# Performance work log

Measured on AMD Instinct MI355X. Metric: run time of the kernel, lower is better.

The kernel has to match this reference:

```python
import jax, jax.numpy as jnp
import numpy as np

HID = 150

def _lstm_layer(x, Wih, Whh, bih, bhh):
    # x: [T, D] -> [T, HID]; PyTorch gate order i, f, g, o
    b = bih + bhh
    xg = x @ Wih.T + b  # precompute input contribution: [T, 4H]
    def step(carry, xg_t):
        h, c = carry
        g = xg_t + h @ Whh.T
        i, f, gg, o = jnp.split(g, 4)
        i = jax.nn.sigmoid(i); f = jax.nn.sigmoid(f)
        gg = jnp.tanh(gg); o = jax.nn.sigmoid(o)
        c = f * c + i * gg
        h = o * jnp.tanh(c)
        return (h, c), h
    init = (jnp.zeros((HID,), x.dtype), jnp.zeros((HID,), x.dtype))
    _, ys = jax.lax.scan(step, init, xg)
    return ys

def _bilstm(x, Wih, Whh, bih, bhh):
    # x: [T, D]; params stacked [L, 2, ...]
    out = x
    for l in range(Wih.shape[0]):
        fwd = _lstm_layer(out, Wih[l, 0], Whh[l, 0], bih[l, 0], bhh[l, 0])
        bwd = _lstm_layer(out[::-1], Wih[l, 1], Whh[l, 1], bih[l, 1], bhh[l, 1])[::-1]
        out = jnp.concatenate([fwd, bwd], axis=-1)  # [T, 2H]
    return out

def setup_inputs() -> dict:
    key = jax.random.key(0)
    ks = jax.random.split(key, 16)
    s = 0.1  # keep LSTM gates in a sane range
    return {
        "inputs_solv": jax.random.normal(ks[0], (1, 4096, 300), jnp.float32),
        "inputs_solu": jax.random.normal(ks[1], (1, 4096, 300), jnp.float32),
        "solv_Wih": jax.random.normal(ks[2], (2, 2, 600, 300), jnp.float32) * s,
        "solv_Whh": jax.random.normal(ks[3], (2, 2, 600, 150), jnp.float32) * s,
        "solv_bih": jax.random.normal(ks[4], (2, 2, 600), jnp.float32) * s,
        "solv_bhh": jax.random.normal(ks[5], (2, 2, 600), jnp.float32) * s,
        "solu_Wih": jax.random.normal(ks[6], (2, 2, 600, 300), jnp.float32) * s,
        "solu_Whh": jax.random.normal(ks[7], (2, 2, 600, 150), jnp.float32) * s,
        "solu_bih": jax.random.normal(ks[8], (2, 2, 600), jnp.float32) * s,
        "solu_bhh": jax.random.normal(ks[9], (2, 2, 600), jnp.float32) * s,
        "fc1_w": jax.random.normal(ks[10], (2000, 600), jnp.float32) * 0.02,
        "fc1_b": jax.random.normal(ks[11], (2000,), jnp.float32) * 0.02,
        "fc2_w": jax.random.normal(ks[12], (1, 2000), jnp.float32) * 0.02,
        "fc2_b": jax.random.normal(ks[13], (1,), jnp.float32) * 0.02,
    }

def reference(inputs_solv, inputs_solu, solv_Wih, solv_Whh, solv_bih, solv_bhh,
              solu_Wih, solu_Whh, solu_bih, solu_bhh, fc1_w, fc1_b, fc2_w, fc2_b):
    H = _bilstm(inputs_solv[0], solv_Wih, solv_Whh, solv_bih, solv_bhh)  # [Hs, 300]
    G = _bilstm(inputs_solu[0], solu_Wih, solu_Whh, solu_bih, solu_bhh)  # [Gs, 300]
    a_score = H @ G.T                      # fused version of the nested loop: [Hs, Gs]
    a = jax.nn.softmax(a_score, axis=1)
    P = a @ G                              # [Hs, 300]
    Q = a.T @ H                            # [Gs, 300]
    u = jnp.maximum(H, P)
    v = jnp.maximum(G, Q)
    inp = jnp.concatenate([u.sum(axis=0), v.sum(axis=0)], axis=0)  # [600]
    x = jax.nn.relu(inp @ fc1_w.T + fc1_b)
    return x @ fc2_w.T + fc2_b
```

## Files before the change

kernel.cpp:

```cpp
#include <hip/hip_runtime.h>
#include <hip/hip_fp16.h>
#include <cstddef>

#define T_LEN 4096
#define HID 150
#define G4 600
#define NC 300

typedef __attribute__((ext_vector_type(8))) short bf16x8;
typedef __attribute__((ext_vector_type(4))) float f32x4;

__device__ __forceinline__ void barrier_lgkm() {
  asm volatile("s_waitcnt lgkmcnt(0)\n\ts_barrier" ::: "memory");
}

__device__ __forceinline__ float fsig(float x) {
  return __builtin_amdgcn_rcpf(1.f + __expf(-x));
}
__device__ __forceinline__ float ftanh(float x) {
  float ax = fabsf(x);
  float e = __expf(2.f * ax);
  float t = 1.f - 2.f * __builtin_amdgcn_rcpf(e + 1.f);
  return copysignf(t, x);
}
__device__ __forceinline__ unsigned short f2bf(float f) {
  unsigned u = __builtin_bit_cast(unsigned, f);
  u += 0x7fff + ((u >> 16) & 1);
  return (unsigned short)(u >> 16);
}

__global__ __launch_bounds__(512, 2) void lstm_scan(
    const float* __restrict__ whh_solv, const float* __restrict__ whh_solu,
    const float* __restrict__ xg_base,
    float* __restrict__ out_solv, float* __restrict__ out_solu, int layer)
{
  __shared__ __align__(16) unsigned short h_bf[160];
  __shared__ float g_s[640];
  const int c = blockIdx.x;
  const int net = c >> 1, dir = c & 1;
  const float* Whh = (net ? whh_solu : whh_solv) + (size_t)(layer * 2 + dir) * (G4 * HID);
  const float* xg = xg_base + (size_t)c * T_LEN * G4;
  float* out = (net ? out_solu : out_solv) + dir * HID;
  const int tid = threadIdx.x;
  const int lane = tid & 63, wv = tid >> 6;
  const int lrow = lane & 15, lq = lane >> 4;

  bf16x8 bfr[5][5];
#pragma unroll
  for (int j = 0; j < 5; j++) {
    const int jrow = 16 * (wv + 8 * j) + lrow;
#pragma unroll
    for (int kk = 0; kk < 5; kk++) {
      bf16x8 b;
#pragma unroll
      for (int i = 0; i < 8; i++) {
        const int k = kk * 32 + lq * 8 + i;
        const float v = (jrow < G4 && k < HID) ? Whh[(size_t)jrow * HID + k] : 0.f;
        b[i] = (short)f2bf(v);
      }
      bfr[j][kk] = b;
    }
  }
  if (tid < 160) h_bf[tid] = 0;
  float cst = 0.f;
  float xr0 = 0.f, xr1 = 0.f, xr2 = 0.f, xr3 = 0.f;
  if (tid < HID) {
    const int t0 = dir ? (T_LEN - 1) : 0;
    const float* xgr = xg + (size_t)t0 * G4 + tid;
    xr0 = xgr[0]; xr1 = xgr[HID]; xr2 = xgr[2 * HID]; xr3 = xgr[3 * HID];
  }
  barrier_lgkm();

  for (int s = 0; s < T_LEN; s++) {
    const int t = dir ? (T_LEN - 1 - s) : s;
    bf16x8 af[5];
#pragma unroll
    for (int kk = 0; kk < 5; kk++) {
      bf16x8 a = {0, 0, 0, 0, 0, 0, 0, 0};
      if (lrow == 0) a = *(const bf16x8*)&h_bf[kk * 32 + lq * 8];
      af[kk] = a;
    }
    f32x4 acc[5];
#pragma unroll
    for (int j = 0; j < 5; j++) acc[j] = (f32x4){0.f, 0.f, 0.f, 0.f};
#pragma unroll
    for (int kk = 0; kk < 5; kk++)
#pragma unroll
      for (int j = 0; j < 5; j++)
        acc[j] = __builtin_amdgcn_mfma_f32_16x16x32_bf16(af[kk], bfr[j][kk], acc[j], 0, 0, 0);
    if (lane < 16) {
#pragma unroll
      for (int j = 0; j < 5; j++) g_s[16 * (wv + 8 * j) + lane] = acc[j][0];
    }
    barrier_lgkm();
    if (tid < HID) {
      const int n = tid;
      float gi = xr0 + g_s[n];
      float gf = xr1 + g_s[HID + n];
      float gg = xr2 + g_s[2 * HID + n];
      float go = xr3 + g_s[3 * HID + n];
      if (s + 1 < T_LEN) {
        const int tn = dir ? (T_LEN - 2 - s) : (s + 1);
        const float* xgr = xg + (size_t)tn * G4 + n;
        xr0 = xgr[0]; xr1 = xgr[HID]; xr2 = xgr[2 * HID]; xr3 = xgr[3 * HID];
      }
      const float iv = fsig(gi), fv = fsig(gf), gv = ftanh(gg), ov = fsig(go);
      cst = fv * cst + iv * gv;
      const float hv = ov * ftanh(cst);
      h_bf[n] = f2bf(hv);
      out[(size_t)t * NC + n] = hv;
    }
    barrier_lgkm();
  }
}

__device__ __forceinline__ float to_f(float v) { return v; }
__device__ __forceinline__ float to_f(__half v) { return __half2float(v); }

#define LP 68

template <int MODE, typename TA, int EPI>
__global__ void gemm_k(const TA* __restrict__ A, const float* __restrict__ B,
                       void* __restrict__ Cv, int M, int N, int K,
                       int lda, int ldb, int ldc,
                       const float* __restrict__ e0, const float* __restrict__ e1)
{
  __shared__ __align__(16) float As[16][LP];
  __shared__ __align__(16) float Bs[16][LP];
  const int tid = threadIdx.x;
  const int tx = tid & 15, ty = tid >> 4;
  const int m0 = blockIdx.y * 64, n0 = blockIdx.x * 64;
  float acc[4][4] = {};
  for (int kc = 0; kc < K; kc += 16) {
#pragma unroll
    for (int j = 0; j < 4; j++) {
      const int li = tid * 4 + j;
      int ml, kl;
      if (MODE == 2) { ml = li & 63; kl = li >> 6; }
      else           { ml = li >> 4; kl = li & 15; }
      const int m = m0 + ml, k = kc + kl;
      float v = 0.f;
      if (m < M && k < K)
        v = to_f(MODE == 2 ? A[(size_t)k * lda + m] : A[(size_t)m * lda + k]);
      As[kl][ml] = v;
    }
#pragma unroll
    for (int j = 0; j < 4; j++) {
      const int li = tid * 4 + j;
      int nl, kl;
      if (MODE == 0) { nl = li >> 4; kl = li & 15; }
      else           { nl = li & 63; kl = li >> 6; }
      const int n = n0 + nl, k = kc + kl;
      float v = 0.f;
      if (n < N && k < K)
        v = (MODE == 0) ? B[(size_t)n * ldb + k] : B[(size_t)k * ldb + n];
      Bs[kl][nl] = v;
    }
    __syncthreads();
#pragma unroll
    for (int kl = 0; kl < 16; kl++) {
      const float4 av = *(const float4*)&As[kl][ty * 4];
      const float4 bv = *(const float4*)&Bs[kl][tx * 4];
      const float aa[4] = {av.x, av.y, av.z, av.w};
      const float bb[4] = {bv.x, bv.y, bv.z, bv.w};
#pragma unroll
      for (int i = 0; i < 4; i++)
#pragma unroll
        for (int jj = 0; jj < 4; jj++)
          acc[i][jj] += aa[i] * bb[jj];
    }
    __syncthreads();
  }
#pragma unroll
  for (int i = 0; i < 4; i++) {
    const int m = m0 + ty * 4 + i;
    if (m >= M) continue;
#pragma unroll
    for (int j = 0; j < 4; j++) {
      const int n = n0 + tx * 4 + j;
      if (n >= N) continue;
      if (EPI == 0) {
        float v = acc[i][j];
        if (e0) v += e0[n] + e1[n];
        ((float*)Cv)[(size_t)m * ldc + n] = v;
      } else {
        const float v = __expf(acc[i][j] - e0[m]) * e1[m];
        ((__half*)Cv)[(size_t)m * ldc + n] = __float2half(v);
      }
    }
  }
}

__global__ void attn_stats(const float* __restrict__ Hm, const float* __restrict__ Gm,
                           float* __restrict__ pm, float* __restrict__ pl)
{
  __shared__ __align__(16) float As[16][LP];
  __shared__ __align__(16) float Bs[16][LP];
  const int tid = threadIdx.x;
  const int tx = tid & 15, ty = tid >> 4;
  const int m0 = blockIdx.y * 64;
  float rm[4], rl[4];
#pragma unroll
  for (int i = 0; i < 4; i++) { rm[i] = -3e38f; rl[i] = 0.f; }
  for (int nt = 0; nt < 8; nt++) {
    const int n0 = (blockIdx.x * 8 + nt) * 64;
    float acc[4][4] = {};
    for (int kc = 0; kc < NC; kc += 16) {
#pragma unroll
      for (int j = 0; j < 4; j++) {
        const int li = tid * 4 + j;
        const int ml = li >> 4, kl = li & 15;
        const int k = kc + kl;
        As[kl][ml] = (k < NC) ? Hm[(size_t)(m0 + ml) * NC + k] : 0.f;
        Bs[kl][ml] = (k < NC) ? Gm[(size_t)(n0 + ml) * NC + k] : 0.f;
      }
      __syncthreads();
#pragma unroll
      for (int kl = 0; kl < 16; kl++) {
        const float4 av = *(const float4*)&As[kl][ty * 4];
        const float4 bv = *(const float4*)&Bs[kl][tx * 4];
        const float aa[4] = {av.x, av.y, av.z, av.w};
        const float bb[4] = {bv.x, bv.y, bv.z, bv.w};
#pragma unroll
        for (int i = 0; i < 4; i++)
#pragma unroll
          for (int jj = 0; jj < 4; jj++)
            acc[i][jj] += aa[i] * bb[jj];
      }
      __syncthreads();
    }
#pragma unroll
    for (int i = 0; i < 4; i++) {
      const float mx = fmaxf(fmaxf(acc[i][0], acc[i][1]), fmaxf(acc[i][2], acc[i][3]));
      const float nm = fmaxf(rm[i], mx);
      const float s = __expf(acc[i][0] - nm) + __expf(acc[i][1] - nm) +
                      __expf(acc[i][2] - nm) + __expf(acc[i][3] - nm);
      rl[i] = rl[i] * __expf(rm[i] - nm) + s;
      rm[i] = nm;
    }
  }
  __syncthreads();
#pragma unroll
  for (int i = 0; i < 4; i++) { As[tx][ty * 4 + i] = rm[i]; Bs[tx][ty * 4 + i] = rl[i]; }
  __syncthreads();
  if (tid < 64) {
    float m = As[0][tid], l = Bs[0][tid];
#pragma unroll
    for (int c2 = 1; c2 < 16; c2++) {
      const float m2 = As[c2][tid], l2 = Bs[c2][tid];
      const float nm = fmaxf(m, m2);
      l = l * __expf(m - nm) + l2 * __expf(m2 - nm);
      m = nm;
    }
    pm[(size_t)(m0 + tid) * 8 + blockIdx.x] = m;
    pl[(size_t)(m0 + tid) * 8 + blockIdx.x] = l;
  }
}

__global__ void stats_combine(const float* __restrict__ pm, const float* __restrict__ pl,
                              float* __restrict__ mrow, float* __restrict__ invl)
{
  const int r = blockIdx.x * 256 + threadIdx.x;
  float m = -3e38f;
#pragma unroll
  for (int c2 = 0; c2 < 8; c2++) m = fmaxf(m, pm[r * 8 + c2]);
  float l = 0.f;
#pragma unroll
  for (int c2 = 0; c2 < 8; c2++) l += pl[r * 8 + c2] * __expf(pm[r * 8 + c2] - m);
  mrow[r] = m;
  invl[r] = 1.f / l;
}

__global__ void zero_inp(float* __restrict__ inp) {
  if (threadIdx.x < 600) inp[threadIdx.x] = 0.f;
}

__global__ void reduce_uv(const float* __restrict__ X, const float* __restrict__ Yp,
                          float* __restrict__ inp, int off)
{
  const int j = threadIdx.x;
  if (j >= NC) return;
  const int r0 = blockIdx.x * 128;
  float s = 0.f;
  for (int r = r0; r < r0 + 128; r++)
    s += fmaxf(X[(size_t)r * NC + j], Yp[(size_t)r * NC + j]);
  atomicAdd(&inp[off + j], s);
}

__global__ void fc1_k(const float* __restrict__ w1, const float* __restrict__ b1,
                      const float* __restrict__ inp, float* __restrict__ x)
{
  const int r = blockIdx.x * 256 + threadIdx.x;
  if (r >= 2000) return;
  float s = b1[r];
  const float* wr = w1 + (size_t)r * 600;
  for (int k = 0; k < 600; k++) s += wr[k] * inp[k];
  x[r] = fmaxf(s, 0.f);
}

__global__ void fc2_k(const float* __restrict__ x, const float* __restrict__ w2,
                      const float* __restrict__ b2, float* __restrict__ outp)
{
  const int tid = threadIdx.x;
  float s = 0.f;
  for (int i = tid; i < 2000; i += 256) s += x[i] * w2[i];
#pragma unroll
  for (int off = 32; off > 0; off >>= 1) s += __shfl_down(s, off);
  __shared__ float red[4];
  if ((tid & 63) == 0) red[tid >> 6] = s;
  __syncthreads();
  if (tid == 0) outp[0] = red[0] + red[1] + red[2] + red[3] + b2[0];
}

extern "C" void kernel_launch(void* const* d_in, const int* in_sizes, int n_in,
                              void* d_out, int out_size, void* d_ws, size_t ws_size,
                              hipStream_t stream)
{
  const float* in_solv  = (const float*)d_in[0];
  const float* in_solu  = (const float*)d_in[1];
  const float* solv_Wih = (const float*)d_in[2];
  const float* solv_Whh = (const float*)d_in[3];
  const float* solv_bih = (const float*)d_in[4];
  const float* solv_bhh = (const float*)d_in[5];
  const float* solu_Wih = (const float*)d_in[6];
  const float* solu_Whh = (const float*)d_in[7];
  const float* solu_bih = (const float*)d_in[8];
  const float* solu_bhh = (const float*)d_in[9];
  const float* fc1_w = (const float*)d_in[10];
  const float* fc1_b = (const float*)d_in[11];
  const float* fc2_w = (const float*)d_in[12];
  const float* fc2_b = (const float*)d_in[13];
  float* outp = (float*)d_out;
  float* ws = (float*)d_ws;

  constexpr size_t off_P   = 0;
  constexpr size_t off_Q   = 1228800;
  constexpr size_t off_inp = 2457600;
  constexpr size_t off_x   = 2458240;
  constexpr size_t off_pm  = 2460288;
  constexpr size_t off_pl  = 2493056;
  constexpr size_t off_mr  = 2525824;
  constexpr size_t off_il  = 2529920;
  constexpr size_t off_xg  = 2534016;
  constexpr size_t off_L0  = off_xg + (size_t)4 * 2457600;
  constexpr size_t off_HG  = off_L0 + (size_t)2 * 1228800;

  float* xg  = ws + off_xg;
  float* L0v = ws + off_L0;
  float* L0u = L0v + 1228800;
  float* Hb  = ws + off_HG;
  float* Gb  = Hb + 1228800;
  float* Pb  = ws + off_P;
  float* Qb  = ws + off_Q;
  float* inp = ws + off_inp;
  float* xf  = ws + off_x;
  float* pm  = ws + off_pm;
  float* pl  = ws + off_pl;
  float* mr  = ws + off_mr;
  float* il  = ws + off_il;
  __half* AH = (__half*)(ws + off_xg);

  for (int c = 0; c < 4; c++) {
    const int net = c >> 1, d = c & 1;
    const float* X   = net ? in_solu : in_solv;
    const float* Wih = (net ? solu_Wih : solv_Wih) + (size_t)d * (600 * 300);
    const float* bi  = (net ? solu_bih : solv_bih) + (size_t)d * 600;
    const float* bh  = (net ? solu_bhh : solv_bhh) + (size_t)d * 600;
    gemm_k<0, float, 0><<<dim3(10, 64), 256, 0, stream>>>(
        X, Wih, (void*)(xg + (size_t)c * 2457600), 4096, 600, 300, 300, 300, 600, bi, bh);
  }
  lstm_scan<<<4, 512, 0, stream>>>(solv_Whh, solu_Whh, xg, L0v, L0u, 0);

  for (int c = 0; c < 4; c++) {
    const int net = c >> 1, d = c & 1;
    const float* X   = net ? L0u : L0v;
    const float* Wih = (net ? solu_Wih : solv_Wih) + (size_t)(2 + d) * (600 * 300);
    const float* bi  = (net ? solu_bih : solv_bih) + (size_t)(2 + d) * 600;
    const float* bh  = (net ? solu_bhh : solv_bhh) + (size_t)(2 + d) * 600;
    gemm_k<0, float, 0><<<dim3(10, 64), 256, 0, stream>>>(
        X, Wih, (void*)(xg + (size_t)c * 2457600), 4096, 600, 300, 300, 300, 600, bi, bh);
  }
  lstm_scan<<<4, 512, 0, stream>>>(solv_Whh, solu_Whh, xg, Hb, Gb, 1);

  attn_stats<<<dim3(8, 64), 256, 0, stream>>>(Hb, Gb, pm, pl);
  stats_combine<<<16, 256, 0, stream>>>(pm, pl, mr, il);
  gemm_k<0, float, 1><<<dim3(64, 64), 256, 0, stream>>>(
      Hb, Gb, (void*)AH, 4096, 4096, 300, 300, 300, 4096, mr, il);
  gemm_k<1, __half, 0><<<dim3(5, 64), 256, 0, stream>>>(
      AH, Gb, (void*)Pb, 4096, 300, 4096, 4096, 300, 300, nullptr, nullptr);
  gemm_k<2, __half, 0><<<dim3(5, 64), 256, 0, stream>>>(
      AH, Hb, (void*)Qb, 4096, 300, 4096, 4096, 300, 300, nullptr, nullptr);

  zero_inp<<<1, 640, 0, stream>>>(inp);
  reduce_uv<<<32, 320, 0, stream>>>(Hb, Pb, inp, 0);
  reduce_uv<<<32, 320, 0, stream>>>(Gb, Qb, inp, 300);
  fc1_k<<<8, 256, 0, stream>>>(fc1_w, fc1_b, inp, xf);
  fc2_k<<<1, 256, 0, stream>>>(xf, fc2_w, fc2_b, outp);
}
```

Measured before the change: 8.071 ms.

## Move input projections and attention GEMMs to fp16 MFMA kernels

Replaces the fp32 SIMT tiled GEMM kernels with fp16 MFMA kernels. One computes the LSTM input projections for all four chains in a single launch. The others handle the attention score, P and Q products, and work on pre-converted, padded or transposed fp16 copies of the weights, inputs and LSTM outputs. The online-max softmax statistics pass is replaced by a fixed shift of 30 with a clamp, followed by an atomic row-sum pass. The recurrent scan also hoists its A-fragment registers out of the step loop and starts accumulation from a zero-accumulator MFMA. This trades fp32 accuracy and the true row-max softmax for tensor-core throughput, and adds several conversion launches. The fixed shift is only safe while attention scores stay in a limited range.

```diff
diff --git a/kernel.cpp b/kernel.cpp
--- a/kernel.cpp
+++ b/kernel.cpp
@@ -8,6 +8,7 @@
 #define NC 300
 
 typedef __attribute__((ext_vector_type(8))) short bf16x8;
+typedef __attribute__((ext_vector_type(8))) _Float16 f16x8;
 typedef __attribute__((ext_vector_type(4))) float f32x4;
 
 __device__ __forceinline__ void barrier_lgkm() {
@@ -69,22 +70,24 @@
     const float* xgr = xg + (size_t)t0 * G4 + tid;
     xr0 = xgr[0]; xr1 = xgr[HID]; xr2 = xgr[2 * HID]; xr3 = xgr[3 * HID];
   }
+  bf16x8 af[5];
+#pragma unroll
+  for (int kk = 0; kk < 5; kk++) af[kk] = (bf16x8){0, 0, 0, 0, 0, 0, 0, 0};
+  const f32x4 z4 = {0.f, 0.f, 0.f, 0.f};
   barrier_lgkm();
 
   for (int s = 0; s < T_LEN; s++) {
     const int t = dir ? (T_LEN - 1 - s) : s;
-    bf16x8 af[5];
-#pragma unroll
-    for (int kk = 0; kk < 5; kk++) {
-      bf16x8 a = {0, 0, 0, 0, 0, 0, 0, 0};
-      if (lrow == 0) a = *(const bf16x8*)&h_bf[kk * 32 + lq * 8];
-      af[kk] = a;
+    if (lrow == 0) {
+#pragma unroll
+      for (int kk = 0; kk < 5; kk++) af[kk] = *(const bf16x8*)&h_bf[kk * 32 + lq * 8];
     }
     f32x4 acc[5];
 #pragma unroll
-    for (int j = 0; j < 5; j++) acc[j] = (f32x4){0.f, 0.f, 0.f, 0.f};
-#pragma unroll
-    for (int kk = 0; kk < 5; kk++)
+    for (int j = 0; j < 5; j++)
+      acc[j] = __builtin_amdgcn_mfma_f32_16x16x32_bf16(af[0], bfr[j][0], z4, 0, 0, 0);
+#pragma unroll
+    for (int kk = 1; kk < 5; kk++)
 #pragma unroll
       for (int j = 0; j < 5; j++)
         acc[j] = __builtin_amdgcn_mfma_f32_16x16x32_bf16(af[kk], bfr[j][kk], acc[j], 0, 0, 0);
@@ -114,165 +117,241 @@
   }
 }
 
-__device__ __forceinline__ float to_f(float v) { return v; }
-__device__ __forceinline__ float to_f(__half v) { return __half2float(v); }
-
-#define LP 68
-
-template <int MODE, typename TA, int EPI>
-__global__ void gemm_k(const TA* __restrict__ A, const float* __restrict__ B,
-                       void* __restrict__ Cv, int M, int N, int K,
-                       int lda, int ldb, int ldc,
-                       const float* __restrict__ e0, const float* __restrict__ e1)
-{
-  __shared__ __align__(16) float As[16][LP];
-  __shared__ __align__(16) float Bs[16][LP];
-  const int tid = threadIdx.x;
-  const int tx = tid & 15, ty = tid >> 4;
-  const int m0 = blockIdx.y * 64, n0 = blockIdx.x * 64;
-  float acc[4][4] = {};
-  for (int kc = 0; kc < K; kc += 16) {
-#pragma unroll
-    for (int j = 0; j < 4; j++) {
-      const int li = tid * 4 + j;
-      int ml, kl;
-      if (MODE == 2) { ml = li & 63; kl = li >> 6; }
-      else           { ml = li >> 4; kl = li & 15; }
-      const int m = m0 + ml, k = kc + kl;
-      float v = 0.f;
-      if (m < M && k < K)
-        v = to_f(MODE == 2 ? A[(size_t)k * lda + m] : A[(size_t)m * lda + k]);
-      As[kl][ml] = v;
-    }
-#pragma unroll
-    for (int j = 0; j < 4; j++) {
-      const int li = tid * 4 + j;
-      int nl, kl;
-      if (MODE == 0) { nl = li >> 4; kl = li & 15; }
-      else           { nl = li & 63; kl = li >> 6; }
-      const int n = n0 + nl, k = kc + kl;
-      float v = 0.f;
-      if (n < N && k < K)
-        v = (MODE == 0) ? B[(size_t)n * ldb + k] : B[(size_t)k * ldb + n];
-      Bs[kl][nl] = v;
-    }
+__global__ void conv_w(const float* __restrict__ wv, const float* __restrict__ wu,
+                       __half* __restrict__ dst)
+{
+  const int gid = blockIdx.x * 256 + threadIdx.x;
+  if (gid >= 8 * 640 * 320) return;
+  const int k = gid % 320, j = (gid / 320) % 640, s = gid / (320 * 640);
+  const int l = s >> 2, net = (s >> 1) & 1, dir = s & 1;
+  float v = 0.f;
+  if (j < G4 && k < NC) {
+    const float* src = (net ? wu : wv) + (size_t)(l * 2 + dir) * (G4 * NC);
+    v = src[(size_t)j * NC + k];
+  }
+  dst[gid] = __float2half(v);
+}
+
+__global__ void conv_x(const float* __restrict__ src, __half* __restrict__ dst, int rows)
+{
+  const int gid = blockIdx.x * 256 + threadIdx.x;
+  if (gid >= rows * 320) return;
+  const int k = gid % 320, m = gid / 320;
+  dst[gid] = __float2half(k < NC ? src[(size_t)m * NC + k] : 0.f);
+}
+
+__global__ void conv_t(const float* __restrict__ src, __half* __restrict__ dst)
+{
+  const int gid = blockIdx.x * 256 + threadIdx.x;
+  if (gid >= 320 * 4096) return;
+  const int m = gid % 4096, f = gid / 4096;
+  dst[gid] = __float2half(f < NC ? src[(size_t)m * NC + f] : 0.f);
+}
+
+__global__ void zero_f(float* __restrict__ p, int n) {
+  const int i = blockIdx.x * 256 + threadIdx.x;
+  if (i < n) p[i] = 0.f;
+}
+
+__global__ __launch_bounds__(256) void xg_mfma(
+    const __half* __restrict__ Av, const __half* __restrict__ Au,
+    const __half* __restrict__ W,
+    const float* __restrict__ bihv, const float* __restrict__ bhhv,
+    const float* __restrict__ bihu, const float* __restrict__ bhhu,
+    float* __restrict__ xg, int layer)
+{
+  const int tid = threadIdx.x;
+  const int lane = tid & 63, wv = tid >> 6;
+  const int ln = lane & 15, q = lane >> 4;
+  const int chain = blockIdx.y;
+  const __half* A = (chain >= 2) ? Au : Av;
+  const __half* Wc = W + (size_t)chain * 640 * 320;
+  const float* bi = ((chain >= 2) ? bihu : bihv) + (size_t)(layer * 2 + (chain & 1)) * G4;
+  const float* bh = ((chain >= 2) ? bhhu : bhhv) + (size_t)(layer * 2 + (chain & 1)) * G4;
+  float* C = xg + (size_t)chain * T_LEN * G4;
+  const int m0 = blockIdx.x * 64 + wv * 16;
+  const __half* Arow = A + (size_t)(m0 + ln) * 320;
+
+  for (int nc = 0; nc < 4; nc++) {
+    f32x4 acc[10];
+#pragma unroll
+    for (int j = 0; j < 10; j++) acc[j] = (f32x4){0.f, 0.f, 0.f, 0.f};
+    for (int kk = 0; kk < 10; kk++) {
+      const f16x8 afr = *(const f16x8*)(Arow + kk * 32 + q * 8);
+#pragma unroll
+      for (int j = 0; j < 10; j++) {
+        const int n = nc * 160 + j * 16 + ln;
+        const f16x8 bfr = *(const f16x8*)(Wc + (size_t)n * 320 + kk * 32 + q * 8);
+        acc[j] = __builtin_amdgcn_mfma_f32_16x16x32_f16(afr, bfr, acc[j], 0, 0, 0);
+      }
+    }
+#pragma unroll
+    for (int j = 0; j < 10; j++) {
+      const int n = nc * 160 + j * 16 + ln;
+      if (n < G4) {
+        const float bias = bi[n] + bh[n];
+#pragma unroll
+        for (int r = 0; r < 4; r++)
+          C[(size_t)(m0 + q * 4 + r) * G4 + n] = acc[j][r] + bias;
+      }
+    }
+  }
+}
+
+__global__ __launch_bounds__(256) void s_pass1(
+    const __half* __restrict__ Hh, const __half* __restrict__ Gh,
+    float* __restrict__ sums)
+{
+  const int tid = threadIdx.x;
+  const int lane = tid & 63, wv = tid >> 6;
+  const int ln = lane & 15, q = lane >> 4;
+  const int m0 = blockIdx.x * 64 + wv * 16;
+  const __half* Arow = Hh + (size_t)(m0 + ln) * 320;
+  f16x8 afr[10];
+#pragma unroll
+  for (int kk = 0; kk < 10; kk++) afr[kk] = *(const f16x8*)(Arow + kk * 32 + q * 8);
+  float rs[4] = {0.f, 0.f, 0.f, 0.f};
+  const int nt0 = blockIdx.y * 64;
+  for (int nt = 0; nt < 64; nt++) {
+    const __half* Brow = Gh + (size_t)(16 * (nt0 + nt) + ln) * 320;
+    f32x4 acc = (f32x4){0.f, 0.f, 0.f, 0.f};
+#pragma unroll
+    for (int kk = 0; kk < 10; kk++) {
+      const f16x8 bfr = *(const f16x8*)(Brow + kk * 32 + q * 8);
+      acc = __builtin_amdgcn_mfma_f32_16x16x32_f16(afr[kk], bfr, acc, 0, 0, 0);
+    }
+#pragma unroll
+    for (int r = 0; r < 4; r++) rs[r] += __expf(fminf(acc[r] - 30.f, 80.f));
+  }
+#pragma unroll
+  for (int m = 1; m <= 8; m <<= 1)
+#pragma unroll
+    for (int r = 0; r < 4; r++) rs[r] += __shfl_xor(rs[r], m);
+  if (ln == 0) {
+#pragma unroll
+    for (int r = 0; r < 4; r++) atomicAdd(&sums[m0 + q * 4 + r], rs[r]);
+  }
+}
+
+__global__ void invert_k(const float* __restrict__ sums, float* __restrict__ il) {
+  const int i = blockIdx.x * 256 + threadIdx.x;
+  if (i < 4096) il[i] = 1.f / sums[i];
+}
+
+__global__ __launch_bounds__(256) void s_pass2(
+    const __half* __restrict__ Hh, const __half* __restrict__ Gh,
+    const float* __restrict__ il, __half* __restrict__ AH)
+{
+  const int tid = threadIdx.x;
+  const int lane = tid & 63, wv = tid >> 6;
+  const int ln = lane & 15, q = lane >> 4;
+  const int m0 = blockIdx.x * 64 + wv * 16;
+  const __half* Arow = Hh + (size_t)(m0 + ln) * 320;
+  f16x8 afr[10];
+#pragma unroll
+  for (int kk = 0; kk < 10; kk++) afr[kk] = *(const f16x8*)(Arow + kk * 32 + q * 8);
+  float ilr[4];
+#pragma unroll
+  for (int r = 0; r < 4; r++) ilr[r] = il[m0 + q * 4 + r];
+  const int nt0 = blockIdx.y * 64;
+  for (int nt = 0; nt < 64; nt++) {
+    const int n = 16 * (nt0 + nt) + ln;
+    const __half* Brow = Gh + (size_t)n * 320;
+    f32x4 acc = (f32x4){0.f, 0.f, 0.f, 0.f};
+#pragma unroll
+    for (int kk = 0; kk < 10; kk++) {
+      const f16x8 bfr = *(const f16x8*)(Brow + kk * 32 + q * 8);
+      acc = __builtin_amdgcn_mfma_f32_16x16x32_f16(afr[kk], bfr, acc, 0, 0, 0);
+    }
+#pragma unroll
+    for (int r = 0; r < 4; r++) {
+      const float a = __expf(fminf(acc[r] - 30.f, 80.f)) * ilr[r];
+      AH[(size_t)(m0 + q * 4 + r) * 4096 + n] = __float2half(a);
+    }
+  }
+}
+
+__global__ __launch_bounds__(256) void p_mfma(
+    const __half* __restrict__ AH, const __half* __restrict__ GhT,
+    float* __restrict__ Pb)
+{
+  const int tid = threadIdx.x;
+  const int lane = tid & 63, wv = tid >> 6;
+  const int ln = lane & 15, q = lane >> 4;
+  const int m0 = blockIdx.x * 64 + wv * 16;
+  const __half* Arow = AH + (size_t)(m0 + ln) * 4096;
+
+  for (int nc = 0; nc < 2; nc++) {
+    f32x4 acc[10];
+#pragma unroll
+    for (int j = 0; j < 10; j++) acc[j] = (f32x4){0.f, 0.f, 0.f, 0.f};
+    for (int kk = 0; kk < 128; kk++) {
+      const f16x8 afr = *(const f16x8*)(Arow + kk * 32 + q * 8);
+#pragma unroll
+      for (int j = 0; j < 10; j++) {
+        const int n = nc * 160 + j * 16 + ln;
+        const f16x8 bfr = *(const f16x8*)(GhT + (size_t)n * 4096 + kk * 32 + q * 8);
+        acc[j] = __builtin_amdgcn_mfma_f32_16x16x32_f16(afr, bfr, acc[j], 0, 0, 0);
+      }
+    }
+#pragma unroll
+    for (int j = 0; j < 10; j++) {
+      const int n = nc * 160 + j * 16 + ln;
+      if (n < NC) {
+#pragma unroll
+        for (int r = 0; r < 4; r++)
+          Pb[(size_t)(m0 + q * 4 + r) * NC + n] = acc[j][r];
+      }
+    }
+  }
+}
+
+__global__ __launch_bounds__(256) void qt_mfma(
+    const __half* __restrict__ AH, const __half* __restrict__ HhT,
+    float* __restrict__ Qb)
+{
+  __shared__ __align__(16) _Float16 Ats[64][72];
+  const int tid = threadIdx.x;
+  const int lane = tid & 63, wv = tid >> 6;
+  const int ln = lane & 15, q = lane >> 4;
+  const int j0 = blockIdx.x * 64;
+  f32x4 acc[20];
+#pragma unroll
+  for (int j = 0; j < 20; j++) acc[j] = (f32x4){0.f, 0.f, 0.f, 0.f};
+  const int il8 = tid >> 2, j8 = (tid & 3) * 16;
+
+  for (int ic = 0; ic < 4096; ic += 64) {
     __syncthreads();
-#pragma unroll
-    for (int kl = 0; kl < 16; kl++) {
-      const float4 av = *(const float4*)&As[kl][ty * 4];
-      const float4 bv = *(const float4*)&Bs[kl][tx * 4];
-      const float aa[4] = {av.x, av.y, av.z, av.w};
-      const float bb[4] = {bv.x, bv.y, bv.z, bv.w};
-#pragma unroll
-      for (int i = 0; i < 4; i++)
-#pragma unroll
-        for (int jj = 0; jj < 4; jj++)
-          acc[i][jj] += aa[i] * bb[jj];
+    {
+      const __half* src = AH + (size_t)(ic + il8) * 4096 + j0 + j8;
+      const f16x8 v0 = *(const f16x8*)src;
+      const f16x8 v1 = *(const f16x8*)(src + 8);
+#pragma unroll
+      for (int jj = 0; jj < 8; jj++) Ats[j8 + jj][il8] = v0[jj];
+#pragma unroll
+      for (int jj = 0; jj < 8; jj++) Ats[j8 + 8 + jj][il8] = v1[jj];
     }
     __syncthreads();
-  }
-#pragma unroll
-  for (int i = 0; i < 4; i++) {
-    const int m = m0 + ty * 4 + i;
-    if (m >= M) continue;
-#pragma unroll
-    for (int j = 0; j < 4; j++) {
-      const int n = n0 + tx * 4 + j;
-      if (n >= N) continue;
-      if (EPI == 0) {
-        float v = acc[i][j];
-        if (e0) v += e0[n] + e1[n];
-        ((float*)Cv)[(size_t)m * ldc + n] = v;
-      } else {
-        const float v = __expf(acc[i][j] - e0[m]) * e1[m];
-        ((__half*)Cv)[(size_t)m * ldc + n] = __float2half(v);
-      }
-    }
-  }
-}
-
-__global__ void attn_stats(const float* __restrict__ Hm, const float* __restrict__ Gm,
-                           float* __restrict__ pm, float* __restrict__ pl)
-{
-  __shared__ __align__(16) float As[16][LP];
-  __shared__ __align__(16) float Bs[16][LP];
-  const int tid = threadIdx.x;
-  const int tx = tid & 15, ty = tid >> 4;
-  const int m0 = blockIdx.y * 64;
-  float rm[4], rl[4];
-#pragma unroll
-  for (int i = 0; i < 4; i++) { rm[i] = -3e38f; rl[i] = 0.f; }
-  for (int nt = 0; nt < 8; nt++) {
-    const int n0 = (blockIdx.x * 8 + nt) * 64;
-    float acc[4][4] = {};
-    for (int kc = 0; kc < NC; kc += 16) {
-#pragma unroll
-      for (int j = 0; j < 4; j++) {
-        const int li = tid * 4 + j;
-        const int ml = li >> 4, kl = li & 15;
-        const int k = kc + kl;
-        As[kl][ml] = (k < NC) ? Hm[(size_t)(m0 + ml) * NC + k] : 0.f;
-        Bs[kl][ml] = (k < NC) ? Gm[(size_t)(n0 + ml) * NC + k] : 0.f;
-      }
-      __syncthreads();
-#pragma unroll
-      for (int kl = 0; kl < 16; kl++) {
-        const float4 av = *(const float4*)&As[kl][ty * 4];
-        const float4 bv = *(const float4*)&Bs[kl][tx * 4];
-        const float aa[4] = {av.x, av.y, av.z, av.w};
-        const float bb[4] = {bv.x, bv.y, bv.z, bv.w};
-#pragma unroll
-        for (int i = 0; i < 4; i++)
-#pragma unroll
-          for (int jj = 0; jj < 4; jj++)
-            acc[i][jj] += aa[i] * bb[jj];
-      }
-      __syncthreads();
-    }
-#pragma unroll
-    for (int i = 0; i < 4; i++) {
-      const float mx = fmaxf(fmaxf(acc[i][0], acc[i][1]), fmaxf(acc[i][2], acc[i][3]));
-      const float nm = fmaxf(rm[i], mx);
-      const float s = __expf(acc[i][0] - nm) + __expf(acc[i][1] - nm) +
-                      __expf(acc[i][2] - nm) + __expf(acc[i][3] - nm);
-      rl[i] = rl[i] * __expf(rm[i] - nm) + s;
-      rm[i] = nm;
-    }
-  }
-  __syncthreads();
-#pragma unroll
-  for (int i = 0; i < 4; i++) { As[tx][ty * 4 + i] = rm[i]; Bs[tx][ty * 4 + i] = rl[i]; }
-  __syncthreads();
-  if (tid < 64) {
-    float m = As[0][tid], l = Bs[0][tid];
-#pragma unroll
-    for (int c2 = 1; c2 < 16; c2++) {
-      const float m2 = As[c2][tid], l2 = Bs[c2][tid];
-      const float nm = fmaxf(m, m2);
-      l = l * __expf(m - nm) + l2 * __expf(m2 - nm);
-      m = nm;
-    }
-    pm[(size_t)(m0 + tid) * 8 + blockIdx.x] = m;
-    pl[(size_t)(m0 + tid) * 8 + blockIdx.x] = l;
-  }
-}
-
-__global__ void stats_combine(const float* __restrict__ pm, const float* __restrict__ pl,
-                              float* __restrict__ mrow, float* __restrict__ invl)
-{
-  const int r = blockIdx.x * 256 + threadIdx.x;
-  float m = -3e38f;
-#pragma unroll
-  for (int c2 = 0; c2 < 8; c2++) m = fmaxf(m, pm[r * 8 + c2]);
-  float l = 0.f;
-#pragma unroll
-  for (int c2 = 0; c2 < 8; c2++) l += pl[r * 8 + c2] * __expf(pm[r * 8 + c2] - m);
-  mrow[r] = m;
-  invl[r] = 1.f / l;
-}
-
-__global__ void zero_inp(float* __restrict__ inp) {
-  if (threadIdx.x < 600) inp[threadIdx.x] = 0.f;
+#pragma unroll
+    for (int s = 0; s < 2; s++) {
+      const f16x8 afr = *(const f16x8*)&Ats[wv * 16 + ln][s * 32 + q * 8];
+      const __half* bbase = HhT + ic + s * 32 + q * 8;
+#pragma unroll
+      for (int j = 0; j < 20; j++) {
+        const f16x8 bfr = *(const f16x8*)(bbase + (size_t)(j * 16 + ln) * 4096);
+        acc[j] = __builtin_amdgcn_mfma_f32_16x16x32_f16(afr, bfr, acc[j], 0, 0, 0);
+      }
+    }
+  }
+#pragma unroll
+  for (int j = 0; j < 20; j++) {
+    const int f = j * 16 + ln;
+    if (f < NC) {
+#pragma unroll
+      for (int r = 0; r < 4; r++)
+        Qb[(size_t)(j0 + wv * 16 + q * 4 + r) * NC + f] = acc[j][r];
+    }
+  }
 }
 
 __global__ void reduce_uv(const float* __restrict__ X, const float* __restrict__ Yp,
@@ -337,61 +416,60 @@
   constexpr size_t off_Q   = 1228800;
   constexpr size_t off_inp = 2457600;
   constexpr size_t off_x   = 2458240;
-  constexpr size_t off_pm  = 2460288;
-  constexpr size_t off_pl  = 2493056;
-  constexpr size_t off_mr  = 2525824;
-  constexpr size_t off_il  = 2529920;
-  constexpr size_t off_xg  = 2534016;
+  constexpr size_t off_il  = 2460288;
+  constexpr size_t off_sm  = 2464384;
+  constexpr size_t off_xg  = 2468480;
   constexpr size_t off_L0  = off_xg + (size_t)4 * 2457600;
   constexpr size_t off_HG  = off_L0 + (size_t)2 * 1228800;
 
-  float* xg  = ws + off_xg;
-  float* L0v = ws + off_L0;
-  float* L0u = L0v + 1228800;
-  float* Hb  = ws + off_HG;
-  float* Gb  = Hb + 1228800;
-  float* Pb  = ws + off_P;
-  float* Qb  = ws + off_Q;
-  float* inp = ws + off_inp;
-  float* xf  = ws + off_x;
-  float* pm  = ws + off_pm;
-  float* pl  = ws + off_pl;
-  float* mr  = ws + off_mr;
-  float* il  = ws + off_il;
-  __half* AH = (__half*)(ws + off_xg);
-
-  for (int c = 0; c < 4; c++) {
-    const int net = c >> 1, d = c & 1;
-    const float* X   = net ? in_solu : in_solv;
-    const float* Wih = (net ? solu_Wih : solv_Wih) + (size_t)d * (600 * 300);
-    const float* bi  = (net ? solu_bih : solv_bih) + (size_t)d * 600;
-    const float* bh  = (net ? solu_bhh : solv_bhh) + (size_t)d * 600;
-    gemm_k<0, float, 0><<<dim3(10, 64), 256, 0, stream>>>(
-        X, Wih, (void*)(xg + (size_t)c * 2457600), 4096, 600, 300, 300, 300, 600, bi, bh);
-  }
+  float*  xg   = ws + off_xg;
+  float*  L0v  = ws + off_L0;
+  float*  L0u  = L0v + 1228800;
+  float*  Hb   = ws + off_HG;
+  float*  Gb   = Hb + 1228800;
+  float*  Pb   = ws + off_P;
+  float*  Qb   = ws + off_Q;
+  float*  inp  = ws + off_inp;
+  float*  xf   = ws + off_x;
+  float*  il   = ws + off_il;
+  float*  sums = ws + off_sm;
+  __half* Wihh = (__half*)(ws + off_P);
+  __half* Avh  = (__half*)(ws + off_L0);
+  __half* Auh  = Avh + 4096 * 320;
+  __half* L0vh = (__half*)(ws + off_HG);
+  __half* L0uh = L0vh + 4096 * 320;
+  __half* Hh   = (__half*)(ws + off_L0);
+  __half* Gh   = Hh + 4096 * 320;
+  __half* AH   = (__half*)(ws + off_xg);
+  __half* HhT  = AH + (size_t)4096 * 4096;
+  __half* GhT  = HhT + 320 * 4096;
+
+  conv_w<<<(8 * 640 * 320 + 255) / 256, 256, 0, stream>>>(solv_Wih, solu_Wih, Wihh);
+  conv_x<<<(4096 * 320 + 255) / 256, 256, 0, stream>>>(in_solv, Avh, 4096);
+  conv_x<<<(4096 * 320 + 255) / 256, 256, 0, stream>>>(in_solu, Auh, 4096);
+
+  xg_mfma<<<dim3(64, 4), 256, 0, stream>>>(Avh, Auh, Wihh,
+      solv_bih, solv_bhh, solu_bih, solu_bhh, xg, 0);
   lstm_scan<<<4, 512, 0, stream>>>(solv_Whh, solu_Whh, xg, L0v, L0u, 0);
 
-  for (int c = 0; c < 4; c++) {
-    const int net = c >> 1, d = c & 1;
-    const float* X   = net ? L0u : L0v;
-    const float* Wih = (net ? solu_Wih : solv_Wih) + (size_t)(2 + d) * (600 * 300);
-    const float* bi  = (net ? solu_bih : solv_bih) + (size_t)(2 + d) * 600;
-    const float* bh  = (net ? solu_bhh : solv_bhh) + (size_t)(2 + d) * 600;
-    gemm_k<0, float, 0><<<dim3(10, 64), 256, 0, stream>>>(
-        X, Wih, (void*)(xg + (size_t)c * 2457600), 4096, 600, 300, 300, 300, 600, bi, bh);
-  }
+  conv_x<<<(4096 * 320 + 255) / 256, 256, 0, stream>>>(L0v, L0vh, 4096);
+  conv_x<<<(4096 * 320 + 255) / 256, 256, 0, stream>>>(L0u, L0uh, 4096);
+  xg_mfma<<<dim3(64, 4), 256, 0, stream>>>(L0vh, L0uh, Wihh + (size_t)4 * 640 * 320,
+      solv_bih, solv_bhh, solu_bih, solu_bhh, xg, 1);
   lstm_scan<<<4, 512, 0, stream>>>(solv_Whh, solu_Whh, xg, Hb, Gb, 1);
 
-  attn_stats<<<dim3(8, 64), 256, 0, stream>>>(Hb, Gb, pm, pl);
-  stats_combine<<<16, 256, 0, stream>>>(pm, pl, mr, il);
-  gemm_k<0, float, 1><<<dim3(64, 64), 256, 0, stream>>>(
-      Hb, Gb, (void*)AH, 4096, 4096, 300, 300, 300, 4096, mr, il);
-  gemm_k<1, __half, 0><<<dim3(5, 64), 256, 0, stream>>>(
-      AH, Gb, (void*)Pb, 4096, 300, 4096, 4096, 300, 300, nullptr, nullptr);
-  gemm_k<2, __half, 0><<<dim3(5, 64), 256, 0, stream>>>(
-      AH, Hb, (void*)Qb, 4096, 300, 4096, 4096, 300, 300, nullptr, nullptr);
-
-  zero_inp<<<1, 640, 0, stream>>>(inp);
+  conv_x<<<(4096 * 320 + 255) / 256, 256, 0, stream>>>(Hb, Hh, 4096);
+  conv_x<<<(4096 * 320 + 255) / 256, 256, 0, stream>>>(Gb, Gh, 4096);
+  conv_t<<<(320 * 4096 + 255) / 256, 256, 0, stream>>>(Hb, HhT);
+  conv_t<<<(320 * 4096 + 255) / 256, 256, 0, stream>>>(Gb, GhT);
+  zero_f<<<16, 256, 0, stream>>>(sums, 4096);
+  s_pass1<<<dim3(64, 4), 256, 0, stream>>>(Hh, Gh, sums);
+  invert_k<<<16, 256, 0, stream>>>(sums, il);
+  s_pass2<<<dim3(64, 4), 256, 0, stream>>>(Hh, Gh, il, AH);
+  p_mfma<<<64, 256, 0, stream>>>(AH, GhT, Pb);
+  qt_mfma<<<64, 256, 0, stream>>>(AH, HhT, Qb);
+
+  zero_f<<<3, 256, 0, stream>>>(inp, 640);
   reduce_uv<<<32, 320, 0, stream>>>(Hb, Pb, inp, 0);
   reduce_uv<<<32, 320, 0, stream>>>(Gb, Qb, inp, 300);
   fc1_k<<<8, 256, 0, stream>>>(fc1_w, fc1_b, inp, xf);
```

Result: faster. 7.672 ms (-4.9%).
